# Optimization experiments

Hardware: AMD Instinct MI355X
Metric: run time of the kernel (lower is better)

The kernel has to match this reference:

```python
import jax, jax.numpy as jnp
import numpy as np

B, S, D, H = 2, 2048, 1024, 16
HD = D // H  # head_dim = 64


def setup_inputs() -> dict:
    key = jax.random.key(0)
    k1, k2, k3, k4, k5 = jax.random.split(key, 5)
    x = jax.random.normal(k1, (B, S, D), dtype=jnp.float32)
    # causal additive mask [S, S]: 0 on/below diagonal, -1e9 above
    mask = jnp.where(jnp.tril(jnp.ones((S, S), dtype=bool)), 0.0, -1e9).astype(jnp.float32)
    scale = 1.0 / np.sqrt(D)
    W_qkv = jax.random.normal(k2, (D, 3 * D), dtype=jnp.float32) * scale
    b_qkv = jax.random.normal(k3, (3 * D,), dtype=jnp.float32) * 0.01
    W_o = jax.random.normal(k4, (D, D), dtype=jnp.float32) * scale
    b_o = jax.random.normal(k5, (D,), dtype=jnp.float32) * 0.01
    return {"x": x, "mask": mask, "W_qkv": W_qkv, "b_qkv": b_qkv, "W_o": W_o, "b_o": b_o}


def reference(x, mask, W_qkv, b_qkv, W_o, b_o):
    b, s, d = x.shape
    qkv = x @ W_qkv + b_qkv                         # [B,S,3D]
    qkv = qkv.reshape(b, s, H, 3 * HD).transpose(0, 2, 1, 3)  # [B,H,S,3*HD]
    q, k, v = jnp.split(qkv, 3, axis=-1)            # each [B,H,S,HD]
    scores = jnp.einsum('bhqd,bhkd->bhqk', q, k) / np.sqrt(HD)  # [B,H,S,S]
    scores = scores + mask                           # broadcast [S,S] additive mask
    attn = jax.nn.softmax(scores, axis=-1)
    vals = jnp.einsum('bhqk,bhkd->bhqd', attn, v)    # [B,H,S,HD]
    vals = vals.transpose(0, 2, 1, 3).reshape(b, s, d)
    return vals @ W_o + b_o
```

## Files before the change

### kernel.cpp

```cpp
#include <hip/hip_runtime.h>

#define NB 2
#define NS 2048
#define ND 1024
#define NH 16
#define NHD 64
#define QLD (3 * ND)
#define PADP 72
#define PADV 68

typedef unsigned short u16;
typedef __attribute__((ext_vector_type(8))) short short8;
typedef __attribute__((ext_vector_type(4))) short short4v;
typedef __attribute__((ext_vector_type(4))) float f32x4;

__device__ __forceinline__ u16 f2b(float f) {
    unsigned int x = __float_as_uint(f);
    return (u16)((x + 0x7fffu + ((x >> 16) & 1u)) >> 16);
}

__device__ __forceinline__ unsigned int cvtpk(float lo, float hi) {
    unsigned int r;
    asm("v_cvt_pk_bf16_f32 %0, %1, %2" : "=v"(r) : "v"(lo), "v"(hi));
    return r;
}

__global__ __launch_bounds__(256) void convert_bf16(
    const float* __restrict__ src, u16* __restrict__ dst, int n)
{
    const int i = (blockIdx.x * 256 + threadIdx.x) * 8;
    if (i >= n) return;
    float4 a = *(const float4*)(src + i);
    float4 b = *(const float4*)(src + i + 4);
    *(ushort4*)(dst + i)     = make_ushort4(f2b(a.x), f2b(a.y), f2b(a.z), f2b(a.w));
    *(ushort4*)(dst + i + 4) = make_ushort4(f2b(b.x), f2b(b.y), f2b(b.z), f2b(b.w));
}

__global__ __launch_bounds__(256) void transpose_bf16(
    const float* __restrict__ W, u16* __restrict__ WT, int K, int N)
{
    __shared__ u16 Ts[64 * 72];
    const int t = threadIdx.x;
    const int k0 = blockIdx.y << 6, n0 = blockIdx.x << 6;
    const int r = t >> 4, c = (t & 15) << 2;
    #pragma unroll
    for (int rr = 0; rr < 64; rr += 16) {
        float4 v = *(const float4*)&W[(size_t)(k0 + r + rr) * N + n0 + c];
        Ts[(c + 0) * 72 + r + rr] = f2b(v.x);
        Ts[(c + 1) * 72 + r + rr] = f2b(v.y);
        Ts[(c + 2) * 72 + r + rr] = f2b(v.z);
        Ts[(c + 3) * 72 + r + rr] = f2b(v.w);
    }
    __syncthreads();
    const int n = t >> 2, cc = (t & 3) << 4;
    uint4 a = *(const uint4*)&Ts[n * 72 + cc];
    uint4 b = *(const uint4*)&Ts[n * 72 + cc + 8];
    *(uint4*)&WT[(size_t)(n0 + n) * K + k0 + cc]     = a;
    *(uint4*)&WT[(size_t)(n0 + n) * K + k0 + cc + 8] = b;
}

template <int BN, bool STORE_BF16>
__global__ __launch_bounds__(256) void gemm_mfma(
    const u16* __restrict__ A, const u16* __restrict__ BT,
    const float* __restrict__ bias,
    void* __restrict__ C, int M, int N, int K)
{
    constexpr int BIS = BN / 64;
    constexpr int NJ  = BN / 32;
    __shared__ u16 As[128 * 32];
    __shared__ u16 Bs[BN * 32];

    const int tid = threadIdx.x;
    const int wave = tid >> 6, lane = tid & 63;
    const int col = lane & 15, quad = lane >> 4;
    const int wm = wave >> 1, wn = wave & 1;
    const int row0 = blockIdx.y << 7, col0 = blockIdx.x * BN;

    f32x4 acc[4][NJ] = {};

    const u16* asrc[2];
    u16* adst[2];
    #pragma unroll
    for (int is = 0; is < 2; ++is) {
        const int J = is * 256 + wave * 64 + lane;
        const int m = J >> 2;
        const int q = (J & 3) ^ ((m >> 1) & 3);
        asrc[is] = A + (size_t)(row0 + m) * K + q * 8;
        adst[is] = &As[(size_t)(is * 256 + wave * 64) * 8];
    }
    const u16* bsrc[BIS];
    u16* bdst[BIS];
    #pragma unroll
    for (int is = 0; is < BIS; ++is) {
        const int J = is * 256 + wave * 64 + lane;
        const int m = J >> 2;
        const int q = (J & 3) ^ ((m >> 1) & 3);
        bsrc[is] = BT + (size_t)(col0 + m) * K + q * 8;
        bdst[is] = &Bs[(size_t)(is * 256 + wave * 64) * 8];
    }

    for (int kk = 0; kk < K; kk += 32) {
        __syncthreads();
        #pragma unroll
        for (int is = 0; is < 2; ++is)
            __builtin_amdgcn_global_load_lds(
                (const __attribute__((address_space(1))) unsigned int*)(asrc[is] + kk),
                (__attribute__((address_space(3))) unsigned int*)adst[is], 16, 0, 0);
        #pragma unroll
        for (int is = 0; is < BIS; ++is)
            __builtin_amdgcn_global_load_lds(
                (const __attribute__((address_space(1))) unsigned int*)(bsrc[is] + kk),
                (__attribute__((address_space(3))) unsigned int*)bdst[is], 16, 0, 0);
        __syncthreads();

        short8 af[4], bf[NJ];
        #pragma unroll
        for (int i = 0; i < 4; ++i) {
            const int m = wm * 64 + i * 16 + col;
            af[i] = *(const short8*)&As[(m * 4 + (quad ^ ((m >> 1) & 3))) * 8];
        }
        #pragma unroll
        for (int j = 0; j < NJ; ++j) {
            const int n = wn * (BN / 2) + j * 16 + col;
            bf[j] = *(const short8*)&Bs[(n * 4 + (quad ^ ((n >> 1) & 3))) * 8];
        }
        #pragma unroll
        for (int i = 0; i < 4; ++i)
            #pragma unroll
            for (int j = 0; j < NJ; ++j)
                acc[i][j] = __builtin_amdgcn_mfma_f32_16x16x32_bf16(
                    af[i], bf[j], acc[i][j], 0, 0, 0);
    }

    #pragma unroll
    for (int j = 0; j < NJ; ++j) {
        const int gc = col0 + wn * (BN / 2) + j * 16 + col;
        const float bj = bias[gc];
        #pragma unroll
        for (int i = 0; i < 4; ++i) {
            const int gr = row0 + wm * 64 + i * 16 + quad * 4;
            #pragma unroll
            for (int r = 0; r < 4; ++r) {
                const float v = acc[i][j][r] + bj;
                if (STORE_BF16)
                    ((u16*)C)[(size_t)(gr + r) * N + gc] = f2b(v);
                else
                    ((float*)C)[(size_t)(gr + r) * N + gc] = v;
            }
        }
    }
}

__global__ __launch_bounds__(256) void attn_kernel(
    const u16* __restrict__ qkv, u16* __restrict__ vals)
{
    __shared__ u16 Ks[2][64 * 64];
    __shared__ u16 Vt[2][64 * PADV];
    __shared__ u16 Ps[2][64 * PADP];

    const int tid = threadIdx.x;
    const int wave = tid >> 6, lane = tid & 63;
    const int col = lane & 15, quad = lane >> 4;
    const int qtA = blockIdx.x;
    const int qtB = 31 - qtA;
    const int bh = blockIdx.y;
    const int b = bh >> 4, h = bh & 15;
    const size_t base = (size_t)b * NS * QLD + (size_t)h * (3 * NHD);
    const int q0 = wave * 16;
    const int qloc = q0 + col;

    int Jrow[2], Jcol[2];
    #pragma unroll
    for (int is = 0; is < 2; ++is) {
        const int J = is * 256 + wave * 64 + lane;
        Jrow[is] = J >> 3;
        Jcol[is] = ((J & 7) ^ (Jrow[is] & 7)) << 3;
    }

    auto stage_tile = [&](int buf, int srow, int coloff) {
        #pragma unroll
        for (int is = 0; is < 2; ++is) {
            __builtin_amdgcn_global_load_lds(
                (const __attribute__((address_space(1))) unsigned int*)
                    (qkv + base + (size_t)(srow + Jrow[is]) * QLD + coloff + Jcol[is]),
                (__attribute__((address_space(3))) unsigned int*)
                    &Ks[buf][(size_t)(is * 256 + wave * 64) * 8], 16, 0, 0);
        }
    };
    auto read_frag = [&](int buf, int row, int half) -> short8 {
        const int blk = row * 8 + ((quad + (half << 2)) ^ (row & 7));
        return *(const short8*)&Ks[buf][blk << 3];
    };

    const int vtx = tid & 15, vty = tid >> 4;
    const int vk0 = vty << 2, vd0 = vtx << 2;
    auto load_vregs = [&](int kt, ushort4* vr) {
        const u16* vsrc = qkv + base + (size_t)(kt * 64 + vk0) * QLD + 2 * NHD + vd0;
        vr[0] = *(const ushort4*)(vsrc);
        vr[1] = *(const ushort4*)(vsrc + QLD);
        vr[2] = *(const ushort4*)(vsrc + 2 * QLD);
        vr[3] = *(const ushort4*)(vsrc + 3 * QLD);
    };
    auto write_vt = [&](int buf, const ushort4* vr) {
        *(ushort4*)&Vt[buf][(vd0 + 0) * PADV + vk0] =
            make_ushort4(vr[0].x, vr[1].x, vr[2].x, vr[3].x);
        *(ushort4*)&Vt[buf][(vd0 + 1) * PADV + vk0] =
            make_ushort4(vr[0].y, vr[1].y, vr[2].y, vr[3].y);
        *(ushort4*)&Vt[buf][(vd0 + 2) * PADV + vk0] =
            make_ushort4(vr[0].z, vr[1].z, vr[2].z, vr[3].z);
        *(ushort4*)&Vt[buf][(vd0 + 3) * PADV + vk0] =
            make_ushort4(vr[0].w, vr[1].w, vr[2].w, vr[3].w);
    };

    stage_tile(0, qtA * 64, 0);
    stage_tile(1, qtB * 64, 0);
    __syncthreads();
    short8 bqA0 = read_frag(0, qloc, 0), bqA1 = read_frag(0, qloc, 1);
    short8 bqB0 = read_frag(1, qloc, 0), bqB1 = read_frag(1, qloc, 1);
    __syncthreads();

    f32x4 accA[4] = {}, accB[4] = {};
    float mA = -1e30f, lA = 0.f, mB = -1e30f, lB = 0.f;

    auto qk = [&](const short8& b0, const short8& b1,
                  short8 (&kb)[4][2], f32x4 (&s)[4]) {
        __builtin_amdgcn_s_setprio(1);
        #pragma unroll
        for (int kg = 0; kg < 4; ++kg) {
            s[kg] = __builtin_amdgcn_mfma_f32_16x16x32_bf16(kb[kg][0], b0, s[kg], 0, 0, 0);
            s[kg] = __builtin_amdgcn_mfma_f32_16x16x32_bf16(kb[kg][1], b1, s[kg], 0, 0, 0);
        }
        __builtin_amdgcn_s_setprio(0);
    };

    auto sm = [&](f32x4 (&s)[4], f32x4 (&accO)[4], float& m, float& l,
                  bool diag, u16* ps) {
        #pragma unroll
        for (int kg = 0; kg < 4; ++kg)
            #pragma unroll
            for (int r = 0; r < 4; ++r) {
                float v = s[kg][r] * 0.125f;
                if (diag && (kg * 16 + quad * 4 + r > qloc)) v = -1e30f;
                s[kg][r] = v;
            }
        float mx = -1e30f;
        #pragma unroll
        for (int kg = 0; kg < 4; ++kg)
            mx = fmaxf(mx, fmaxf(fmaxf(s[kg][0], s[kg][1]), fmaxf(s[kg][2], s[kg][3])));
        mx = fmaxf(mx, __shfl_xor(mx, 16, 64));
        mx = fmaxf(mx, __shfl_xor(mx, 32, 64));
        if (!__all(mx <= m + 8.f)) {
            const float mn = fmaxf(m, mx);
            const float alpha = __expf(m - mn);
            m = mn;
            l *= alpha;
            #pragma unroll
            for (int dg = 0; dg < 4; ++dg)
                #pragma unroll
                for (int r = 0; r < 4; ++r) accO[dg][r] *= alpha;
        }
        float psum = 0.f;
        #pragma unroll
        for (int kg = 0; kg < 4; ++kg) {
            float p0 = __expf(s[kg][0] - m);
            float p1 = __expf(s[kg][1] - m);
            float p2 = __expf(s[kg][2] - m);
            float p3 = __expf(s[kg][3] - m);
            psum += (p0 + p1) + (p2 + p3);
            uint2 w;
            w.x = cvtpk(p0, p1);
            w.y = cvtpk(p2, p3);
            *(uint2*)&ps[qloc * PADP + kg * 16 + quad * 4] = w;
        }
        psum += __shfl_xor(psum, 16, 64);
        psum += __shfl_xor(psum, 32, 64);
        l += psum;
    };

    auto pv = [&](short8 (&vb)[4][2], f32x4 (&accO)[4], const u16* ps) {
        short8 pb0 = *(const short8*)&ps[qloc * PADP + quad * 8];
        short8 pb1 = *(const short8*)&ps[qloc * PADP + 32 + quad * 8];
        __builtin_amdgcn_s_setprio(1);
        #pragma unroll
        for (int dg = 0; dg < 4; ++dg) {
            accO[dg] = __builtin_amdgcn_mfma_f32_16x16x32_bf16(vb[dg][0], pb0, accO[dg], 0, 0, 0);
            accO[dg] = __builtin_amdgcn_mfma_f32_16x16x32_bf16(vb[dg][1], pb1, accO[dg], 0, 0, 0);
        }
        __builtin_amdgcn_s_setprio(0);
    };

    ushort4 vcur[4], vnxt[4];
    stage_tile(0, 0, NHD);
    load_vregs(0, vcur);

    for (int kt = 0; kt <= qtB; ++kt) {
        const int cur = kt & 1, nxt = cur ^ 1;
        __syncthreads();
        write_vt(cur, vcur);
        __syncthreads();
        if (kt < qtB) {
            stage_tile(nxt, (kt + 1) * 64, NHD);
            load_vregs(kt + 1, vnxt);
        }

        short8 kb[4][2], vb[4][2];
        #pragma unroll
        for (int kg = 0; kg < 4; ++kg) {
            kb[kg][0] = read_frag(cur, kg * 16 + col, 0);
            kb[kg][1] = read_frag(cur, kg * 16 + col, 1);
        }
        #pragma unroll
        for (int dg = 0; dg < 4; ++dg) {
            const int n = dg * 16 + col;
            short4v lo0 = *(const short4v*)&Vt[cur][n * PADV + quad * 8];
            short4v hi0 = *(const short4v*)&Vt[cur][n * PADV + quad * 8 + 4];
            short4v lo1 = *(const short4v*)&Vt[cur][n * PADV + 32 + quad * 8];
            short4v hi1 = *(const short4v*)&Vt[cur][n * PADV + 32 + quad * 8 + 4];
            vb[dg][0] = __builtin_shufflevector(lo0, hi0, 0, 1, 2, 3, 4, 5, 6, 7);
            vb[dg][1] = __builtin_shufflevector(lo1, hi1, 0, 1, 2, 3, 4, 5, 6, 7);
        }

        if (kt <= qtA) {
            f32x4 sB[4] = {}, sA[4] = {};
            qk(bqB0, bqB1, kb, sB);
            qk(bqA0, bqA1, kb, sA);
            sm(sB, accB, mB, lB, false, Ps[0]);
            sm(sA, accA, mA, lA, kt == qtA, Ps[1]);
            pv(vb, accB, Ps[0]);
            pv(vb, accA, Ps[1]);
        } else {
            f32x4 sB[4] = {};
            qk(bqB0, bqB1, kb, sB);
            sm(sB, accB, mB, lB, kt == qtB, Ps[0]);
            pv(vb, accB, Ps[0]);
        }

        #pragma unroll
        for (int i = 0; i < 4; ++i) vcur[i] = vnxt[i];
    }

    {
        const float inv = 1.f / lA;
        const size_t rowoff = ((size_t)b * NS + qtA * 64 + qloc) * ND + h * NHD;
        #pragma unroll
        for (int dg = 0; dg < 4; ++dg) {
            uint2 o;
            o.x = cvtpk(accA[dg][0] * inv, accA[dg][1] * inv);
            o.y = cvtpk(accA[dg][2] * inv, accA[dg][3] * inv);
            *(uint2*)(vals + rowoff + dg * 16 + quad * 4) = o;
        }
    }
    {
        const float inv = 1.f / lB;
        const size_t rowoff = ((size_t)b * NS + qtB * 64 + qloc) * ND + h * NHD;
        #pragma unroll
        for (int dg = 0; dg < 4; ++dg) {
            uint2 o;
            o.x = cvtpk(accB[dg][0] * inv, accB[dg][1] * inv);
            o.y = cvtpk(accB[dg][2] * inv, accB[dg][3] * inv);
            *(uint2*)(vals + rowoff + dg * 16 + quad * 4) = o;
        }
    }
}

extern "C" void kernel_launch(void* const* d_in, const int* in_sizes, int n_in,
                              void* d_out, int out_size, void* d_ws, size_t ws_size,
                              hipStream_t stream)
{
    const float* x    = (const float*)d_in[0];
    const float* Wqkv = (const float*)d_in[2];
    const float* bqkv = (const float*)d_in[3];
    const float* Wo   = (const float*)d_in[4];
    const float* bo   = (const float*)d_in[5];
    float* out = (float*)d_out;

    u16* x_bf   = (u16*)d_ws;
    u16* WqkvT  = x_bf   + (size_t)4096 * 1024;
    u16* WoT    = WqkvT  + (size_t)3072 * 1024;
    u16* qkv    = WoT    + (size_t)1024 * 1024;
    u16* vals   = qkv    + (size_t)4096 * 3072;

    const int M = NB * NS;

    convert_bf16<<<dim3(M * ND / (256 * 8)), dim3(256), 0, stream>>>(
        x, x_bf, M * ND);
    transpose_bf16<<<dim3(QLD / 64, ND / 64), dim3(256), 0, stream>>>(
        Wqkv, WqkvT, ND, QLD);
    transpose_bf16<<<dim3(ND / 64, ND / 64), dim3(256), 0, stream>>>(
        Wo, WoT, ND, ND);

    gemm_mfma<128, true><<<dim3(QLD / 128, M / 128), dim3(256), 0, stream>>>(
        x_bf, WqkvT, bqkv, qkv, M, QLD, ND);
    attn_kernel<<<dim3(16, NB * NH), dim3(256), 0, stream>>>(qkv, vals);
    gemm_mfma<64, false><<<dim3(ND / 64, M / 128), dim3(256), 0, stream>>>(
        vals, WoT, bo, out, M, ND, ND);
}
```

Baseline: 220.0 us.

## Fuse prep kernels, swizzle GEMM tiles, drop attention barrier and P buffer

Merges the x conversion and the two weight transposes into one prep launch whose blocks dispatch on blockIdx. Adds a workgroup-index swizzle to the GEMM so consecutive tiles are spread across groups of eight. In attention, the V transpose for the next tile is written at the end of each iteration, which removes one __syncthreads per key tile. Attention also now uses a single P staging buffer and runs the two query tiles one after the other instead of interleaving them, lowering LDS use but giving less MFMA/softmax overlap between the two tiles.

Result: faster. 210.8 us (-4.2%).

```diff
diff --git a/kernel.cpp b/kernel.cpp
--- a/kernel.cpp
+++ b/kernel.cpp
@@ -25,31 +25,42 @@
     return r;
 }
 
-__global__ __launch_bounds__(256) void convert_bf16(
-    const float* __restrict__ src, u16* __restrict__ dst, int n)
-{
-    const int i = (blockIdx.x * 256 + threadIdx.x) * 8;
-    if (i >= n) return;
-    float4 a = *(const float4*)(src + i);
-    float4 b = *(const float4*)(src + i + 4);
-    *(ushort4*)(dst + i)     = make_ushort4(f2b(a.x), f2b(a.y), f2b(a.z), f2b(a.w));
-    *(ushort4*)(dst + i + 4) = make_ushort4(f2b(b.x), f2b(b.y), f2b(b.z), f2b(b.w));
-}
-
-__global__ __launch_bounds__(256) void transpose_bf16(
-    const float* __restrict__ W, u16* __restrict__ WT, int K, int N)
+__global__ __launch_bounds__(256) void prep(
+    const float* __restrict__ x, u16* __restrict__ x_bf,
+    const float* __restrict__ Wqkv, u16* __restrict__ WqkvT,
+    const float* __restrict__ Wo, u16* __restrict__ WoT)
 {
     __shared__ u16 Ts[64 * 72];
+    const int bid = blockIdx.x;
     const int t = threadIdx.x;
-    const int k0 = blockIdx.y << 6, n0 = blockIdx.x << 6;
-    const int r = t >> 4, c = (t & 15) << 2;
+
+    if (bid < 2048) {
+        const int i = (bid * 256 + t) * 8;
+        float4 a = *(const float4*)(x + i);
+        float4 b = *(const float4*)(x + i + 4);
+        *(ushort4*)(x_bf + i)     = make_ushort4(f2b(a.x), f2b(a.y), f2b(a.z), f2b(a.w));
+        *(ushort4*)(x_bf + i + 4) = make_ushort4(f2b(b.x), f2b(b.y), f2b(b.z), f2b(b.w));
+        return;
+    }
+
+    const float* W; u16* WT; int N, bx, by;
+    if (bid < 2048 + 768) {
+        const int r = bid - 2048;
+        W = Wqkv; WT = WqkvT; N = QLD; bx = r % 48; by = r / 48;
+    } else {
+        const int r = bid - 2816;
+        W = Wo; WT = WoT; N = ND; bx = r & 15; by = r >> 4;
+    }
+    const int K = ND;
+    const int k0 = by << 6, n0 = bx << 6;
+    const int rr0 = t >> 4, c = (t & 15) << 2;
     #pragma unroll
     for (int rr = 0; rr < 64; rr += 16) {
-        float4 v = *(const float4*)&W[(size_t)(k0 + r + rr) * N + n0 + c];
-        Ts[(c + 0) * 72 + r + rr] = f2b(v.x);
-        Ts[(c + 1) * 72 + r + rr] = f2b(v.y);
-        Ts[(c + 2) * 72 + r + rr] = f2b(v.z);
-        Ts[(c + 3) * 72 + r + rr] = f2b(v.w);
+        float4 v = *(const float4*)&W[(size_t)(k0 + rr0 + rr) * N + n0 + c];
+        Ts[(c + 0) * 72 + rr0 + rr] = f2b(v.x);
+        Ts[(c + 1) * 72 + rr0 + rr] = f2b(v.y);
+        Ts[(c + 2) * 72 + rr0 + rr] = f2b(v.z);
+        Ts[(c + 3) * 72 + rr0 + rr] = f2b(v.w);
     }
     __syncthreads();
     const int n = t >> 2, cc = (t & 3) << 4;
@@ -74,7 +85,12 @@
     const int wave = tid >> 6, lane = tid & 63;
     const int col = lane & 15, quad = lane >> 4;
     const int wm = wave >> 1, wn = wave & 1;
-    const int row0 = blockIdx.y << 7, col0 = blockIdx.x * BN;
+
+    const int nwgx = gridDim.x;
+    const int wg = blockIdx.y * nwgx + blockIdx.x;
+    const int cpx = (nwgx * gridDim.y) >> 3;
+    const int swz = (wg & 7) * cpx + (wg >> 3);
+    const int row0 = (swz / nwgx) << 7, col0 = (swz % nwgx) * BN;
 
     f32x4 acc[4][NJ] = {};
 
@@ -156,7 +172,7 @@
 {
     __shared__ u16 Ks[2][64 * 64];
     __shared__ u16 Vt[2][64 * PADV];
-    __shared__ u16 Ps[2][64 * PADP];
+    __shared__ u16 Ps[64 * PADP];
 
     const int tid = threadIdx.x;
     const int wave = tid >> 6, lane = tid & 63;
@@ -166,8 +182,7 @@
     const int bh = blockIdx.y;
     const int b = bh >> 4, h = bh & 15;
     const size_t base = (size_t)b * NS * QLD + (size_t)h * (3 * NHD);
-    const int q0 = wave * 16;
-    const int qloc = q0 + col;
+    const int qloc = wave * 16 + col;
 
     int Jrow[2], Jcol[2];
     #pragma unroll
@@ -233,8 +248,7 @@
         __builtin_amdgcn_s_setprio(0);
     };
 
-    auto sm = [&](f32x4 (&s)[4], f32x4 (&accO)[4], float& m, float& l,
-                  bool diag, u16* ps) {
+    auto sm = [&](f32x4 (&s)[4], f32x4 (&acc)[4], float& m, float& l, bool diag) {
         #pragma unroll
         for (int kg = 0; kg < 4; ++kg)
             #pragma unroll
@@ -257,7 +271,7 @@
             #pragma unroll
             for (int dg = 0; dg < 4; ++dg)
                 #pragma unroll
-                for (int r = 0; r < 4; ++r) accO[dg][r] *= alpha;
+                for (int r = 0; r < 4; ++r) acc[dg][r] *= alpha;
         }
         float psum = 0.f;
         #pragma unroll
@@ -270,37 +284,36 @@
             uint2 w;
             w.x = cvtpk(p0, p1);
             w.y = cvtpk(p2, p3);
-            *(uint2*)&ps[qloc * PADP + kg * 16 + quad * 4] = w;
+            *(uint2*)&Ps[qloc * PADP + kg * 16 + quad * 4] = w;
         }
         psum += __shfl_xor(psum, 16, 64);
         psum += __shfl_xor(psum, 32, 64);
         l += psum;
     };
 
-    auto pv = [&](short8 (&vb)[4][2], f32x4 (&accO)[4], const u16* ps) {
-        short8 pb0 = *(const short8*)&ps[qloc * PADP + quad * 8];
-        short8 pb1 = *(const short8*)&ps[qloc * PADP + 32 + quad * 8];
+    auto pv = [&](short8 (&vb)[4][2], f32x4 (&acc)[4]) {
+        short8 pb0 = *(const short8*)&Ps[qloc * PADP + quad * 8];
+        short8 pb1 = *(const short8*)&Ps[qloc * PADP + 32 + quad * 8];
         __builtin_amdgcn_s_setprio(1);
         #pragma unroll
         for (int dg = 0; dg < 4; ++dg) {
-            accO[dg] = __builtin_amdgcn_mfma_f32_16x16x32_bf16(vb[dg][0], pb0, accO[dg], 0, 0, 0);
-            accO[dg] = __builtin_amdgcn_mfma_f32_16x16x32_bf16(vb[dg][1], pb1, accO[dg], 0, 0, 0);
+            acc[dg] = __builtin_amdgcn_mfma_f32_16x16x32_bf16(vb[dg][0], pb0, acc[dg], 0, 0, 0);
+            acc[dg] = __builtin_amdgcn_mfma_f32_16x16x32_bf16(vb[dg][1], pb1, acc[dg], 0, 0, 0);
         }
         __builtin_amdgcn_s_setprio(0);
     };
 
-    ushort4 vcur[4], vnxt[4];
+    ushort4 vr[4];
     stage_tile(0, 0, NHD);
-    load_vregs(0, vcur);
+    load_vregs(0, vr);
+    write_vt(0, vr);
 
     for (int kt = 0; kt <= qtB; ++kt) {
         const int cur = kt & 1, nxt = cur ^ 1;
         __syncthreads();
-        write_vt(cur, vcur);
-        __syncthreads();
         if (kt < qtB) {
             stage_tile(nxt, (kt + 1) * 64, NHD);
-            load_vregs(kt + 1, vnxt);
+            load_vregs(kt + 1, vr);
         }
 
         short8 kb[4][2], vb[4][2];
@@ -320,23 +333,20 @@
             vb[dg][1] = __builtin_shufflevector(lo1, hi1, 0, 1, 2, 3, 4, 5, 6, 7);
         }
 
+        {
+            f32x4 s[4] = {};
+            qk(bqB0, bqB1, kb, s);
+            sm(s, accB, mB, lB, kt == qtB);
+            pv(vb, accB);
+        }
         if (kt <= qtA) {
-            f32x4 sB[4] = {}, sA[4] = {};
-            qk(bqB0, bqB1, kb, sB);
-            qk(bqA0, bqA1, kb, sA);
-            sm(sB, accB, mB, lB, false, Ps[0]);
-            sm(sA, accA, mA, lA, kt == qtA, Ps[1]);
-            pv(vb, accB, Ps[0]);
-            pv(vb, accA, Ps[1]);
-        } else {
-            f32x4 sB[4] = {};
-            qk(bqB0, bqB1, kb, sB);
-            sm(sB, accB, mB, lB, kt == qtB, Ps[0]);
-            pv(vb, accB, Ps[0]);
-        }
-
-        #pragma unroll
-        for (int i = 0; i < 4; ++i) vcur[i] = vnxt[i];
+            f32x4 s[4] = {};
+            qk(bqA0, bqA1, kb, s);
+            sm(s, accA, mA, lA, kt == qtA);
+            pv(vb, accA);
+        }
+
+        if (kt < qtB) write_vt(nxt, vr);
     }
 
     {
@@ -382,12 +392,8 @@
 
     const int M = NB * NS;
 
-    convert_bf16<<<dim3(M * ND / (256 * 8)), dim3(256), 0, stream>>>(
-        x, x_bf, M * ND);
-    transpose_bf16<<<dim3(QLD / 64, ND / 64), dim3(256), 0, stream>>>(
-        Wqkv, WqkvT, ND, QLD);
-    transpose_bf16<<<dim3(ND / 64, ND / 64), dim3(256), 0, stream>>>(
-        Wo, WoT, ND, ND);
+    prep<<<dim3(2048 + 768 + 256), dim3(256), 0, stream>>>(
+        x, x_bf, Wqkv, WqkvT, Wo, WoT);
 
     gemm_mfma<128, true><<<dim3(QLD / 128, M / 128), dim3(256), 0, stream>>>(
         x_bf, WqkvT, bqkv, qkv, M, QLD, ND);
```
